# Optimization experiments

Hardware: AMD Instinct MI355X
Metric: run time of the kernel (lower is better)

The kernel has to match this reference:

```python
import jax, jax.numpy as jnp
import numpy as np

D, DFFN, H, P, L = 256, 1024, 8, 4, 4
B, LQ = 32, 300
LENS = [2048, 1024, 512, 256]
STARTS = [0, 2048, 3072, 3584]
S = sum(LENS)


def setup_inputs() -> dict:
    key = jax.random.key(0)
    ks = iter(jax.random.split(key, 64))
    def W(shape, s=0.02):
        return jax.random.normal(next(ks), shape, jnp.float32) * s
    inp = {}
    inp['tgt'] = W((B, LQ, D), 1.0)
    inp['query_pos'] = W((B, LQ, D), 1.0)
    centers = jax.random.uniform(next(ks), (B, LQ, L))
    widths = 0.05 + 0.2 * jax.random.uniform(next(ks), (B, LQ, L))
    inp['reference_points'] = jnp.stack([centers, widths], -1)  # (B,Lq,L,2) = (center,width)
    inp['src'] = W((B, S, D), 1.0)
    inp['temporal_lengths'] = np.array(LENS, np.int64)
    inp['level_start_index'] = np.array(STARTS, np.int64)
    for n, shape in [('sa_qw', (D, D)), ('sa_kw', (D, D)), ('sa_vw', (D, D)), ('sa_ow', (D, D)), ('ff1_w', (D, DFFN)), ('ff2_w', (DFFN, D))]:
        inp[n] = W(shape)
    for n, sz in [('sa_qb', D), ('sa_kb', D), ('sa_vb', D), ('sa_ob', D), ('ff1_b', DFFN), ('ff2_b', D)]:
        inp[n] = jnp.zeros((sz,), jnp.float32)
    for pre in ['ca', 'se']:
        inp[pre + '_off_w'] = W((D, H * L * P))
        inp[pre + '_off_b'] = jnp.zeros((H * L * P,), jnp.float32)
        inp[pre + '_attn_w'] = W((D, H * L * P))
        inp[pre + '_attn_b'] = jnp.zeros((H * L * P,), jnp.float32)
        inp[pre + '_val_w'] = W((D, D))
        inp[pre + '_val_b'] = jnp.zeros((D,), jnp.float32)
        inp[pre + '_out_w'] = W((D, D))
        inp[pre + '_out_b'] = jnp.zeros((D,), jnp.float32)
    for n in ['ln1', 'lnse', 'ln2', 'ln3']:
        inp[n + '_g'] = jnp.ones((D,), jnp.float32)
        inp[n + '_b'] = jnp.zeros((D,), jnp.float32)
    return inp


def _ln(x, g, b, eps=1e-5):
    m = jnp.mean(x, -1, keepdims=True)
    v = jnp.mean((x - m) ** 2, -1, keepdims=True)
    return (x - m) * jax.lax.rsqrt(v + eps) * g + b


def _mha(q, k, v, qw, qb, kw, kb, vw, vb, ow, ob):
    b, lq, d = q.shape
    dh = d // H
    qh = (q @ qw + qb).reshape(b, lq, H, dh).transpose(0, 2, 1, 3)
    kh = (k @ kw + kb).reshape(b, -1, H, dh).transpose(0, 2, 1, 3)
    vh = (v @ vw + vb).reshape(b, -1, H, dh).transpose(0, 2, 1, 3)
    scores = jnp.einsum('bhqd,bhkd->bhqk', qh, kh) * (dh ** -0.5)
    attn = jax.nn.softmax(scores, -1)
    out = jnp.einsum('bhqk,bhkd->bhqd', attn, vh).transpose(0, 2, 1, 3).reshape(b, lq, d)
    return out @ ow + ob


def _deform(q, ref, src, lens, starts, vw, vb, offw, offb, aw, ab, ow, ob, boundary):
    b, lq, d = q.shape
    dh = d // H
    value = (src @ vw + vb).reshape(b, -1, H, dh)  # (B,S,H,Dh)
    off = (q @ offw + offb).reshape(b, lq, H, L, P)
    attn = jax.nn.softmax((q @ aw + ab).reshape(b, lq, H, L * P), -1).reshape(b, lq, H, L, P)
    center = ref[..., 0][:, :, None, :, None]  # (B,Lq,1,L,1)
    width = ref[..., 1][:, :, None, :, None]
    if boundary:
        # half the points anchored at segment start, half at segment end
        sign = jnp.where(jnp.arange(P) < P // 2, -0.5, 0.5)
        anchor = center + sign * width
    else:
        anchor = center
    loc = anchor + off / P * width * 0.5  # normalized sampling locations (B,Lq,H,L,P)
    out = jnp.zeros((b, lq, H, dh), value.dtype)
    for l in range(L):
        T = int(lens[l]); s0 = int(starts[l])
        v = value[:, s0:s0 + T].transpose(0, 2, 1, 3)  # (B,H,T,Dh)
        x = loc[:, :, :, l, :] * T - 0.5  # align_corners=False grid
        x0 = jnp.floor(x)
        w = x - x0
        i0 = x0.astype(jnp.int32)
        i1 = i0 + 1
        m0 = ((i0 >= 0) & (i0 < T)).astype(v.dtype)
        m1 = ((i1 >= 0) & (i1 < T)).astype(v.dtype)
        i0c = jnp.clip(i0, 0, T - 1)
        i1c = jnp.clip(i1, 0, T - 1)
        def gather(idx):
            idxh = idx.transpose(0, 2, 1, 3).reshape(b, H, lq * P, 1)
            g = jnp.take_along_axis(v, jnp.broadcast_to(idxh, (b, H, lq * P, dh)), axis=2)
            return g.reshape(b, H, lq, P, dh).transpose(0, 2, 1, 3, 4)  # (B,Lq,H,P,Dh)
        samp = gather(i0c) * ((1 - w) * m0)[..., None] + gather(i1c) * (w * m1)[..., None]
        out = out + jnp.einsum('bqhp,bqhpd->bqhd', attn[:, :, :, l, :], samp)
    return out.reshape(b, lq, d) @ ow + ob


def reference(tgt, query_pos, reference_points, src, temporal_lengths, level_start_index,
              sa_qw, sa_qb, sa_kw, sa_kb, sa_vw, sa_vb, sa_ow, sa_ob,
              ca_off_w, ca_off_b, ca_attn_w, ca_attn_b, ca_val_w, ca_val_b, ca_out_w, ca_out_b,
              se_off_w, se_off_b, se_attn_w, se_attn_b, se_val_w, se_val_b, se_out_w, se_out_b,
              ff1_w, ff1_b, ff2_w, ff2_b,
              ln1_g, ln1_b, lnse_g, lnse_b, ln2_g, ln2_b, ln3_g, ln3_b):
    lens = np.asarray(temporal_lengths)
    starts = np.asarray(level_start_index)
    q = tgt + query_pos
    t2 = _mha(q, q, tgt, sa_qw, sa_qb, sa_kw, sa_kb, sa_vw, sa_vb, sa_ow, sa_ob)
    tgt = _ln(tgt + t2, ln2_g, ln2_b)
    t2 = _deform(tgt + query_pos, reference_points, src, lens, starts,
                 ca_val_w, ca_val_b, ca_off_w, ca_off_b, ca_attn_w, ca_attn_b, ca_out_w, ca_out_b, False)
    tgt = _ln(tgt + t2, ln1_g, ln1_b)
    t2 = _deform(tgt + query_pos, reference_points, src, lens, starts,
                 se_val_w, se_val_b, se_off_w, se_off_b, se_attn_w, se_attn_b, se_out_w, se_out_b, True)
    tgt = _ln(tgt + t2, lnse_g, lnse_b)
    t2 = jax.nn.relu(tgt @ ff1_w + ff1_b) @ ff2_w + ff2_b
    tgt = _ln(tgt + t2, ln3_g, ln3_b)
    return tgt
```

## Files before the change

kernel.cpp:

```cpp
#include <hip/hip_runtime.h>
#include <hip/hip_bf16.h>

namespace {

typedef unsigned short u16;
typedef unsigned int u32;

constexpr int D    = 256;
constexpr int H    = 8;
constexpr int DH   = 32;
constexpr int L    = 4;
constexpr int P    = 4;
constexpr int B    = 32;
constexpr int LQ   = 300;
constexpr int NQ   = B * LQ;
constexpr int S    = 3840;
constexpr int MS   = B * S;
constexpr int DFFN = 1024;

typedef __attribute__((ext_vector_type(8))) short bf16x8;
typedef __attribute__((ext_vector_type(4))) float f32x4;

__device__ inline u16 f2b(float x) {
  u32 u = __builtin_bit_cast(u32, x);
  u32 r = (u + 0x7FFFu + ((u >> 16) & 1u)) >> 16;
  return (u16)r;
}
__device__ inline u32 pk2(float a, float b) {
  return (u32)f2b(a) | ((u32)f2b(b) << 16);
}
__device__ inline void unpack2(u32 w, float& a, float& b) {
  a = __builtin_bit_cast(float, w << 16);
  b = __builtin_bit_cast(float, w & 0xffff0000u);
}

template<bool OUT_BF16, bool RELU>
__global__ __launch_bounds__(256) void gemm_sm(
    const u16* __restrict__ A, const u16* __restrict__ Bt,
    const float* __restrict__ bias, void* __restrict__ Cv,
    int M, int K, int N)
{
  constexpr int BM = 64, BN = 64, BK = 64, LDK = 72;
  __shared__ __align__(16) u16 sh[(BM + BN) * LDK];
  u16* As = sh;
  u16* Bs = sh + BM * LDK;
  const int tid  = threadIdx.x;
  const int lane = tid & 63;
  const int wid  = tid >> 6;
  const int wm = wid >> 1, wn = wid & 1;
  const int m0 = blockIdx.y * BM, n0 = blockIdx.x * BN;

  f32x4 acc[2][2] = {};
  uint4 ra[2], rb[2];
  const int NT = K / BK;
  const int srow = tid >> 3, sch = (tid & 7) * 8;

#pragma unroll
  for (int i = 0; i < 2; ++i) {
    const int row = srow + i * 32;
    ra[i] = *(const uint4*)(A  + (size_t)(m0 + row) * K + sch);
    rb[i] = *(const uint4*)(Bt + (size_t)(n0 + row) * K + sch);
  }

  for (int t = 0; t < NT; ++t) {
#pragma unroll
    for (int i = 0; i < 2; ++i) {
      const int row = srow + i * 32;
      *(uint4*)(&As[row * LDK + sch]) = ra[i];
      *(uint4*)(&Bs[row * LDK + sch]) = rb[i];
    }
    __syncthreads();
    if (t + 1 < NT) {
      const int k0 = (t + 1) * BK;
#pragma unroll
      for (int i = 0; i < 2; ++i) {
        const int row = srow + i * 32;
        ra[i] = *(const uint4*)(A  + (size_t)(m0 + row) * K + k0 + sch);
        rb[i] = *(const uint4*)(Bt + (size_t)(n0 + row) * K + k0 + sch);
      }
    }
#pragma unroll
    for (int kk = 0; kk < 2; ++kk) {
      const int krd = kk * 32 + (lane >> 4) * 8;
      bf16x8 af[2], bf[2];
#pragma unroll
      for (int m = 0; m < 2; ++m)
        af[m] = *(const bf16x8*)(&As[(wm * 32 + (lane & 15) + 16 * m) * LDK + krd]);
#pragma unroll
      for (int n = 0; n < 2; ++n)
        bf[n] = *(const bf16x8*)(&Bs[(wn * 32 + (lane & 15) + 16 * n) * LDK + krd]);
#pragma unroll
      for (int m = 0; m < 2; ++m)
#pragma unroll
        for (int n = 0; n < 2; ++n)
          acc[m][n] = __builtin_amdgcn_mfma_f32_16x16x32_bf16(af[m], bf[n], acc[m][n], 0, 0, 0);
    }
    __syncthreads();
  }

  const int cr = (lane >> 4) * 4;
  const int cc = lane & 15;
  if constexpr (OUT_BF16) {
    u16* stg = sh;
#pragma unroll
    for (int n = 0; n < 2; ++n) {
      const int lc = wn * 32 + n * 16 + cc;
      const float bv = bias[n0 + lc];
#pragma unroll
      for (int m = 0; m < 2; ++m) {
        const int lr0 = wm * 32 + m * 16 + cr;
#pragma unroll
        for (int r = 0; r < 4; ++r) {
          float x = acc[m][n][r] + bv;
          if (RELU) x = fmaxf(x, 0.f);
          stg[(lr0 + r) * LDK + lc] = f2b(x);
        }
      }
    }
    __syncthreads();
    u16* Cb = (u16*)Cv;
#pragma unroll
    for (int i = 0; i < 2; ++i) {
      const int c = tid + 256 * i;
      const int row = c >> 3, ch = c & 7;
      *(uint4*)(Cb + (size_t)(m0 + row) * N + n0 + ch * 8) =
          *(const uint4*)(&stg[row * LDK + ch * 8]);
    }
  } else {
#pragma unroll
    for (int n = 0; n < 2; ++n) {
      const int gc = n0 + wn * 32 + n * 16 + cc;
      const float bv = bias[gc];
#pragma unroll
      for (int m = 0; m < 2; ++m) {
        const int gr0 = m0 + wm * 32 + m * 16 + cr;
#pragma unroll
        for (int r = 0; r < 4; ++r) {
          float x = acc[m][n][r] + bv;
          if (RELU) x = fmaxf(x, 0.f);
          ((float*)Cv)[(size_t)(gr0 + r) * N + gc] = x;
        }
      }
    }
  }
}

__global__ __launch_bounds__(256) void gemm_qkv(
    const u16* __restrict__ qbuf, const u16* __restrict__ tgtb,
    const u16* __restrict__ saqk_t, const u16* __restrict__ sav_t,
    const float* __restrict__ qkb, const float* __restrict__ vbias,
    u16* __restrict__ qkbuf, u16* __restrict__ vh)
{
  constexpr int K = 256, BK = 64, LDK = 72;
  __shared__ __align__(16) u16 sh[128 * LDK];
  u16* As = sh;
  u16* Bs = sh + 64 * LDK;
  const bool isv = blockIdx.x >= 8;
  const u16* A  = isv ? tgtb : qbuf;
  const u16* Bt = isv ? sav_t : saqk_t;
  const float* bias = isv ? vbias : qkb;
  u16* C = isv ? vh : qkbuf;
  const int N = isv ? 256 : 512;
  const int n0 = (isv ? (int)blockIdx.x - 8 : (int)blockIdx.x) * 64;
  const int m0 = blockIdx.y * 64;

  const int tid  = threadIdx.x;
  const int lane = tid & 63;
  const int wid  = tid >> 6;
  const int wm = wid >> 1, wn = wid & 1;

  f32x4 acc[2][2] = {};
  uint4 ra[2], rb[2];
  const int srow = tid >> 3, sch = (tid & 7) * 8;

#pragma unroll
  for (int i = 0; i < 2; ++i) {
    const int row = srow + i * 32;
    ra[i] = *(const uint4*)(A  + (size_t)(m0 + row) * K + sch);
    rb[i] = *(const uint4*)(Bt + (size_t)(n0 + row) * K + sch);
  }
  for (int t = 0; t < 4; ++t) {
#pragma unroll
    for (int i = 0; i < 2; ++i) {
      const int row = srow + i * 32;
      *(uint4*)(&As[row * LDK + sch]) = ra[i];
      *(uint4*)(&Bs[row * LDK + sch]) = rb[i];
    }
    __syncthreads();
    if (t + 1 < 4) {
      const int k0 = (t + 1) * BK;
#pragma unroll
      for (int i = 0; i < 2; ++i) {
        const int row = srow + i * 32;
        ra[i] = *(const uint4*)(A  + (size_t)(m0 + row) * K + k0 + sch);
        rb[i] = *(const uint4*)(Bt + (size_t)(n0 + row) * K + k0 + sch);
      }
    }
#pragma unroll
    for (int kk = 0; kk < 2; ++kk) {
      const int krd = kk * 32 + (lane >> 4) * 8;
      bf16x8 af[2], bf[2];
#pragma unroll
      for (int m = 0; m < 2; ++m)
        af[m] = *(const bf16x8*)(&As[(wm * 32 + (lane & 15) + 16 * m) * LDK + krd]);
#pragma unroll
      for (int n = 0; n < 2; ++n)
        bf[n] = *(const bf16x8*)(&Bs[(wn * 32 + (lane & 15) + 16 * n) * LDK + krd]);
#pragma unroll
      for (int m = 0; m < 2; ++m)
#pragma unroll
        for (int n = 0; n < 2; ++n)
          acc[m][n] = __builtin_amdgcn_mfma_f32_16x16x32_bf16(af[m], bf[n], acc[m][n], 0, 0, 0);
    }
    __syncthreads();
  }

  const int cr = (lane >> 4) * 4;
  const int cc = lane & 15;
  u16* stg = sh;
#pragma unroll
  for (int n = 0; n < 2; ++n) {
    const int lc = wn * 32 + n * 16 + cc;
    const float bv = bias[n0 + lc];
#pragma unroll
    for (int m = 0; m < 2; ++m) {
      const int lr0 = wm * 32 + m * 16 + cr;
#pragma unroll
      for (int r = 0; r < 4; ++r)
        stg[(lr0 + r) * LDK + lc] = f2b(acc[m][n][r] + bv);
    }
  }
  __syncthreads();
#pragma unroll
  for (int i = 0; i < 2; ++i) {
    const int c = tid + 256 * i;
    const int row = c >> 3, ch = c & 7;
    *(uint4*)(C + (size_t)(m0 + row) * N + n0 + ch * 8) =
        *(const uint4*)(&stg[row * LDK + ch * 8]);
  }
}

__global__ __launch_bounds__(512) void gemm_val4(
    const float* __restrict__ A, const u16* __restrict__ Bt2,
    const float* __restrict__ bias2, u16* __restrict__ Vca, u16* __restrict__ Vse)
{
  __shared__ __align__(16) char shraw[33792];
  char* Asw = shraw;
  const int tid  = threadIdx.x;
  const int lane = tid & 63;
  const int w    = tid >> 6;
  const int nh   = blockIdx.x & 1;
  const int m0   = (blockIdx.x >> 1) * 64;
  u16* dst = nh ? Vse : Vca;
  const u16* Bt = Bt2 + nh * 256 * 256;
  const float* bias = bias2 + nh * 256;

#pragma unroll
  for (int i = 0; i < 4; ++i) {
    const int idx = tid + 512 * i;
    const int row = idx >> 5, ch = idx & 31;
    const float* ap = A + (size_t)(m0 + row) * 256 + ch * 8;
    const float4 f0 = *(const float4*)(ap);
    const float4 f1 = *(const float4*)(ap + 4);
    uint4 pk;
    pk.x = pk2(f0.x, f0.y); pk.y = pk2(f0.z, f0.w);
    pk.z = pk2(f1.x, f1.y); pk.w = pk2(f1.z, f1.w);
    *(uint4*)(Asw + row * 512 + ((ch * 16) ^ ((row & 7) << 4))) = pk;
  }
  __syncthreads();

  f32x4 acc[4][2] = {};
  const u16* bb = Bt + (size_t)(w * 32 + (lane & 15)) * 256 + (lane >> 4) * 8;
  bf16x8 bcur[2], bnxt[2];
#pragma unroll
  for (int n = 0; n < 2; ++n) bcur[n] = *(const bf16x8*)(bb + n * 4096);

#pragma unroll
  for (int kk = 0; kk < 8; ++kk) {
    bf16x8 af[4];
    const int kb = kk * 64 + (lane >> 4) * 16;
#pragma unroll
    for (int m = 0; m < 4; ++m) {
      const int row = m * 16 + (lane & 15);
      af[m] = *(const bf16x8*)(Asw + row * 512 + (kb ^ ((row & 7) << 4)));
    }
    if (kk < 7) {
#pragma unroll
      for (int n = 0; n < 2; ++n)
        bnxt[n] = *(const bf16x8*)(bb + n * 4096 + (kk + 1) * 32);
    }
#pragma unroll
    for (int m = 0; m < 4; ++m)
#pragma unroll
      for (int n = 0; n < 2; ++n)
        acc[m][n] = __builtin_amdgcn_mfma_f32_16x16x32_bf16(af[m], bcur[n], acc[m][n], 0, 0, 0);
#pragma unroll
    for (int n = 0; n < 2; ++n) bcur[n] = bnxt[n];
  }
  __syncthreads();

  constexpr int STC = 264;
  u16* stg = (u16*)shraw;
  const int cr = (lane >> 4) * 4;
  const int cc = lane & 15;
#pragma unroll
  for (int n = 0; n < 2; ++n) {
    const int col = w * 32 + n * 16 + cc;
    const float bv = bias[col];
#pragma unroll
    for (int m = 0; m < 4; ++m) {
      const int r0 = m * 16 + cr;
#pragma unroll
      for (int r = 0; r < 4; ++r)
        stg[(r0 + r) * STC + col] = f2b(acc[m][n][r] + bv);
    }
  }
  __syncthreads();
#pragma unroll
  for (int i = 0; i < 4; ++i) {
    const int c = tid + 512 * i;
    const int row = c >> 5, ch = c & 31;
    *(uint4*)(dst + (size_t)(m0 + row) * 256 + ch * 8) =
        *(const uint4*)(&stg[row * STC + ch * 8]);
  }
}

template<int MODE>
__global__ __launch_bounds__(1024) void gemm_ln(
    const u16* __restrict__ A, const u16* __restrict__ Bt,
    const float* __restrict__ bias, const float* __restrict__ res,
    const float* __restrict__ g, const float* __restrict__ be,
    const float* __restrict__ qpos,
    float* __restrict__ fout, u16* __restrict__ bfout, int K)
{
  constexpr int BK = 64, LDK = 72;
  __shared__ __align__(16) float ftile[64 * 264];
  u16* As = (u16*)ftile;
  u16* Bs = As + 64 * LDK;
  const int tid  = threadIdx.x;
  const int lane = tid & 63;
  const int wid  = tid >> 6;
  const int wm = wid >> 2, wn = wid & 3;
  const int m0 = blockIdx.x * 64;

  f32x4 acc[4] = {};
  const int NT = K / BK;
  const bool am = tid < 512;
  const int arow = tid >> 3, ach = (tid & 7) * 8;

  uint4 ra = {};
  uint4 rb[2];
  if (am) ra = *(const uint4*)(A + (size_t)(m0 + arow) * K + ach);
#pragma unroll
  for (int i = 0; i < 2; ++i) {
    const int idx = tid + 1024 * i;
    const int brow = idx >> 3, bch = (idx & 7) * 8;
    rb[i] = *(const uint4*)(Bt + (size_t)brow * K + bch);
  }

  for (int t = 0; t < NT; ++t) {
    if (am) *(uint4*)(&As[arow * LDK + ach]) = ra;
#pragma unroll
    for (int i = 0; i < 2; ++i) {
      const int idx = tid + 1024 * i;
      const int brow = idx >> 3, bch = (idx & 7) * 8;
      *(uint4*)(&Bs[brow * LDK + bch]) = rb[i];
    }
    __syncthreads();
    if (t + 1 < NT) {
      const int k0 = (t + 1) * BK;
      if (am) ra = *(const uint4*)(A + (size_t)(m0 + arow) * K + k0 + ach);
#pragma unroll
      for (int i = 0; i < 2; ++i) {
        const int idx = tid + 1024 * i;
        const int brow = idx >> 3, bch = (idx & 7) * 8;
        rb[i] = *(const uint4*)(Bt + (size_t)brow * K + k0 + bch);
      }
    }
#pragma unroll
    for (int kk = 0; kk < 2; ++kk) {
      const int krd = kk * 32 + (lane >> 4) * 8;
      bf16x8 af, bf[4];
      af = *(const bf16x8*)(&As[(wm * 16 + (lane & 15)) * LDK + krd]);
#pragma unroll
      for (int n = 0; n < 4; ++n)
        bf[n] = *(const bf16x8*)(&Bs[(wn * 64 + n * 16 + (lane & 15)) * LDK + krd]);
#pragma unroll
      for (int n = 0; n < 4; ++n)
        acc[n] = __builtin_amdgcn_mfma_f32_16x16x32_bf16(af, bf[n], acc[n], 0, 0, 0);
    }
    __syncthreads();
  }

  const int cr = (lane >> 4) * 4;
  const int cc = lane & 15;
#pragma unroll
  for (int n = 0; n < 4; ++n) {
    const int col = wn * 64 + n * 16 + cc;
    const float bv = bias[col];
#pragma unroll
    for (int r = 0; r < 4; ++r)
      ftile[(wm * 16 + cr + r) * 264 + col] = acc[n][r] + bv;
  }
  __syncthreads();

  const int row = tid >> 4, s16 = tid & 15;
  const size_t grow = (size_t)(m0 + row) * 256;
  float vv[16];
  float sum = 0.f;
#pragma unroll
  for (int j = 0; j < 4; ++j) {
    const int col = s16 * 4 + j * 64;
    const float4 fv = *(const float4*)(&ftile[row * 264 + col]);
    const float4 rv = *(const float4*)(res + grow + col);
    vv[j * 4 + 0] = fv.x + rv.x; vv[j * 4 + 1] = fv.y + rv.y;
    vv[j * 4 + 2] = fv.z + rv.z; vv[j * 4 + 3] = fv.w + rv.w;
    sum += vv[j * 4 + 0] + vv[j * 4 + 1] + vv[j * 4 + 2] + vv[j * 4 + 3];
  }
  sum += __shfl_xor(sum, 1, 64);
  sum += __shfl_xor(sum, 2, 64);
  sum += __shfl_xor(sum, 4, 64);
  sum += __shfl_xor(sum, 8, 64);
  const float mean = sum * (1.f / 256.f);
  float sq = 0.f;
#pragma unroll
  for (int k = 0; k < 16; ++k) { const float d = vv[k] - mean; sq += d * d; }
  sq += __shfl_xor(sq, 1, 64);
  sq += __shfl_xor(sq, 2, 64);
  sq += __shfl_xor(sq, 4, 64);
  sq += __shfl_xor(sq, 8, 64);
  const float rstd = rsqrtf(sq * (1.f / 256.f) + 1e-5f);

#pragma unroll
  for (int j = 0; j < 4; ++j) {
    const int col = s16 * 4 + j * 64;
    const float4 gv = *(const float4*)(g + col);
    const float4 bv = *(const float4*)(be + col);
    float4 y;
    y.x = (vv[j * 4 + 0] - mean) * rstd * gv.x + bv.x;
    y.y = (vv[j * 4 + 1] - mean) * rstd * gv.y + bv.y;
    y.z = (vv[j * 4 + 2] - mean) * rstd * gv.z + bv.z;
    y.w = (vv[j * 4 + 3] - mean) * rstd * gv.w + bv.w;
    *(float4*)(fout + grow + col) = y;
    if constexpr (MODE == 0) {
      const float4 qv = *(const float4*)(qpos + grow + col);
      uint2 pk;
      pk.x = pk2(y.x + qv.x, y.y + qv.y);
      pk.y = pk2(y.z + qv.z, y.w + qv.w);
      *(uint2*)(bfout + grow + col) = pk;
    } else if constexpr (MODE == 1) {
      uint2 pk;
      pk.x = pk2(y.x, y.y);
      pk.y = pk2(y.z, y.w);
      *(uint2*)(bfout + grow + col) = pk;
    }
  }
}

struct WSpec { const float* w; u16* wt; int K, N, blk0; };
struct WPack { WSpec s[14]; };

struct PrepArgs {
  const float *ca_off_b, *ca_attn_b, *se_off_b, *se_attn_b;
  const float *sa_qb, *sa_kb, *ca_val_b, *se_val_b;
  float *bias4, *qkb, *valb;
  const float *tgt, *qpos;
  u16 *tgtb, *qbuf;
  int n4, nwt;
};

__global__ __launch_bounds__(256) void prep_all(WPack p, PrepArgs a) {
  __shared__ float tile[32][33];
  const int b = blockIdx.x;
  if (b < a.nwt) {
    int i = 0;
#pragma unroll
    for (int j = 1; j < 14; ++j) if (b >= p.s[j].blk0) i = j;
    const float* w = p.s[i].w;
    u16* wt = p.s[i].wt;
    const int K = p.s[i].K, N = p.s[i].N;
    const int lb = b - p.s[i].blk0;
    const int ntN = N >> 5;
    const int tk = lb / ntN, tn = lb - tk * ntN;
    const int r = threadIdx.x >> 5, c = threadIdx.x & 31;
#pragma unroll
    for (int j = 0; j < 4; ++j)
      tile[r + j * 8][c] = w[(size_t)(tk * 32 + r + j * 8) * N + tn * 32 + c];
    __syncthreads();
#pragma unroll
    for (int j = 0; j < 4; ++j)
      wt[(size_t)(tn * 32 + r + j * 8) * K + tk * 32 + c] = f2b(tile[c][r + j * 8]);
  } else if (b == a.nwt) {
#pragma unroll
    for (int u = 0; u < 2; ++u) {
      const int t = threadIdx.x + 256 * u;
      a.bias4[t] = t < 128 ? a.ca_off_b[t] : t < 256 ? a.ca_attn_b[t - 128]
                 : t < 384 ? a.se_off_b[t - 256] : a.se_attn_b[t - 384];
      a.qkb[t]  = t < 256 ? a.sa_qb[t] : a.sa_kb[t - 256];
      a.valb[t] = t < 256 ? a.ca_val_b[t] : a.se_val_b[t - 256];
    }
  } else {
    const int i = (b - a.nwt - 1) * 256 + threadIdx.x;
    if (i < a.n4) {
      const float4 t = ((const float4*)a.tgt)[i];
      const float4 q = ((const float4*)a.qpos)[i];
      uint2 x, y;
      x.x = pk2(t.x, t.y); x.y = pk2(t.z, t.w);
      y.x = pk2(t.x + q.x, t.y + q.y); y.y = pk2(t.z + q.z, t.w + q.w);
      ((uint2*)a.tgtb)[i] = x;
      ((uint2*)a.qbuf)[i] = y;
    }
  }
}

__global__ __launch_bounds__(512) void mha_v2(
    const u16* __restrict__ qk, const u16* __restrict__ vh,
    u16* __restrict__ out)
{
  __shared__ __align__(16) float Ks[8 * 300 * 4];
  __shared__ __align__(16) float Vs[8 * 300 * 4];
  const int bh  = blockIdx.x & 255;
  const int seg = blockIdx.x >> 8;
  const int b = bh >> 3, h = bh & 7;
  const u16* kbase = qk + (size_t)b * LQ * 512 + 256 + h * DH;
  const u16* vbase = vh + (size_t)b * LQ * D + h * DH;
  for (int e = threadIdx.x; e < 300 * 8; e += 512) {
    const int r = e >> 3, j = e & 7;
    float4 f;
    const uint2 kv = *(const uint2*)(kbase + (size_t)r * 512 + j * 4);
    unpack2(kv.x, f.x, f.y);
    unpack2(kv.y, f.z, f.w);
    *(float4*)(&Ks[(j * 300 + r) * 4]) = f;
    const uint2 vv = *(const uint2*)(vbase + (size_t)r * D + j * 4);
    unpack2(vv.x, f.x, f.y);
    unpack2(vv.y, f.z, f.w);
    *(float4*)(&Vs[(j * 300 + r) * 4]) = f;
  }
  __syncthreads();

  const int lane = threadIdx.x & 63;
  const int lq = (threadIdx.x >> 6) * 16 + (lane >> 2);
  const int kc = lane & 3;
  const int q = seg * 128 + lq;
  if (q >= LQ) return;

  const u16* qrow = qk + (size_t)(b * LQ + q) * 512 + h * DH;
  float qv[DH];
#pragma unroll
  for (int c4 = 0; c4 < 4; ++c4) {
    const uint4 u = *(const uint4*)(qrow + c4 * 8);
    unpack2(u.x, qv[c4 * 8 + 0], qv[c4 * 8 + 1]);
    unpack2(u.y, qv[c4 * 8 + 2], qv[c4 * 8 + 3]);
    unpack2(u.z, qv[c4 * 8 + 4], qv[c4 * 8 + 5]);
    unpack2(u.w, qv[c4 * 8 + 6], qv[c4 * 8 + 7]);
  }
#pragma unroll
  for (int d = 0; d < DH; ++d) qv[d] *= 0.17677669529663689f;

  float o[DH] = {};
  float ssum = 0.f;
  const float* kp = &Ks[kc * 75 * 4];
  const float* vp = &Vs[kc * 75 * 4];
  for (int i = 0; i < 75; ++i) {
    float s = 0.f;
#pragma unroll
    for (int j = 0; j < 8; ++j) {
      const float4 kf = *(const float4*)(kp + i * 4 + j * 1200);
      s += qv[j * 4 + 0] * kf.x + qv[j * 4 + 1] * kf.y
         + qv[j * 4 + 2] * kf.z + qv[j * 4 + 3] * kf.w;
    }
    const float p = __expf(s);
    ssum += p;
#pragma unroll
    for (int j = 0; j < 8; ++j) {
      const float4 vf = *(const float4*)(vp + i * 4 + j * 1200);
      o[j * 4 + 0] += p * vf.x; o[j * 4 + 1] += p * vf.y;
      o[j * 4 + 2] += p * vf.z; o[j * 4 + 3] += p * vf.w;
    }
  }

  ssum += __shfl_xor(ssum, 1, 64);
  ssum += __shfl_xor(ssum, 2, 64);
#pragma unroll
  for (int d = 0; d < DH; ++d) {
    o[d] += __shfl_xor(o[d], 1, 64);
    o[d] += __shfl_xor(o[d], 2, 64);
  }
  const float inv = 1.f / ssum;

  u16* orow = out + (size_t)(b * LQ + q) * D + h * DH;
#pragma unroll
  for (int c = 0; c < 4; ++c) {
    if (kc == c) {
      uint4 w;
      w.x = pk2(o[c * 8 + 0] * inv, o[c * 8 + 1] * inv);
      w.y = pk2(o[c * 8 + 2] * inv, o[c * 8 + 3] * inv);
      w.z = pk2(o[c * 8 + 4] * inv, o[c * 8 + 5] * inv);
      w.w = pk2(o[c * 8 + 6] * inv, o[c * 8 + 7] * inv);
      *(uint4*)(orow + c * 8) = w;
    }
  }
}

template<bool BOUNDARY>
__global__ __launch_bounds__(512) void deform_v2(
    const float* __restrict__ oa, const float* __restrict__ ref,
    const u16* __restrict__ value, u16* __restrict__ out)
{
  __shared__ __align__(16) uint4 owt[4][128];
  const int unit = threadIdx.x >> 7;
  const int bq = blockIdx.x * 4 + unit;
  const int b = bq / LQ;
  const int t = threadIdx.x & 127;
  const int h = t >> 4;
  const int l = (t >> 2) & 3;
  const int p = t & 3;

  const float off   = oa[(size_t)bq * 256 + t];
  const float logit = oa[(size_t)bq * 256 + 128 + t];
  const float center = ref[(size_t)bq * 8 + l * 2 + 0];
  const float width  = ref[(size_t)bq * 8 + l * 2 + 1];

  const float e = __expf(logit);
  float ssum = e;
  ssum += __shfl_xor(ssum, 1, 64);
  ssum += __shfl_xor(ssum, 2, 64);
  ssum += __shfl_xor(ssum, 4, 64);
  ssum += __shfl_xor(ssum, 8, 64);
  const float wa = e / ssum;

  const int T  = 2048 >> l;
  const int s0 = 4096 - (4096 >> l);
  float anchor = center;
  if (BOUNDARY) anchor += (p < 2 ? -0.5f : 0.5f) * width;
  const float loc = anchor + off * width * 0.125f;
  const float x = loc * (float)T - 0.5f;
  const float x0 = floorf(x);
  const float w = x - x0;
  const int i0 = (int)x0;
  const int i1 = i0 + 1;
  const float w0 = (i0 >= 0 && i0 < T) ? wa * (1.f - w) : 0.f;
  const float w1 = (i1 >= 0 && i1 < T) ? wa * w : 0.f;
  const int i0c = min(max(i0, 0), T - 1);
  const int i1c = min(max(i1, 0), T - 1);
  uint4 pack;
  pack.x = (u32)((s0 + i0c) * (D * 2) + h * (DH * 2));
  pack.y = __builtin_bit_cast(u32, w0);
  pack.z = (u32)((s0 + i1c) * (D * 2) + h * (DH * 2));
  pack.w = __builtin_bit_cast(u32, w1);
  owt[unit][t] = pack;
  __syncthreads();

  const int g  = t >> 4;
  const int ln = t & 15;
  const char* vb = (const char*)(value + (size_t)b * S * D) + ln * 4;
  float o0 = 0.f, o1 = 0.f;
#pragma unroll
  for (int j = 0; j < 16; ++j) {
    const uint4 ow = owt[unit][g * 16 + j];
    const u32 v0 = *(const u32*)(vb + ow.x);
    const u32 v1 = *(const u32*)(vb + ow.z);
    const float wt0 = __builtin_bit_cast(float, ow.y);
    const float wt1 = __builtin_bit_cast(float, ow.w);
    float a, c;
    unpack2(v0, a, c); o0 += wt0 * a; o1 += wt0 * c;
    unpack2(v1, a, c); o0 += wt1 * a; o1 += wt1 * c;
  }
  const u32 res = pk2(o0, o1);
  *(u32*)(out + (size_t)bq * D + g * DH + ln * 2) = res;
}

}

extern "C" void kernel_launch(void* const* d_in, const int* in_sizes, int n_in,
                              void* d_out, int out_size, void* d_ws, size_t ws_size,
                              hipStream_t stream)
{
  const float* tgt   = (const float*)d_in[0];
  const float* qpos  = (const float*)d_in[1];
  const float* ref   = (const float*)d_in[2];
  const float* src   = (const float*)d_in[3];
  const float* sa_qw = (const float*)d_in[6];
  const float* sa_kw = (const float*)d_in[7];
  const float* sa_vw = (const float*)d_in[8];
  const float* sa_ow = (const float*)d_in[9];
  const float* ff1_w = (const float*)d_in[10];
  const float* ff2_w = (const float*)d_in[11];
  const float* sa_qb = (const float*)d_in[12];
  const float* sa_kb = (const float*)d_in[13];
  const float* sa_vb = (const float*)d_in[14];
  const float* sa_ob = (const float*)d_in[15];
  const float* ff1_b = (const float*)d_in[16];
  const float* ff2_b = (const float*)d_in[17];
  const float* ca_off_w  = (const float*)d_in[18];
  const float* ca_off_b  = (const float*)d_in[19];
  const float* ca_attn_w = (const float*)d_in[20];
  const float* ca_attn_b = (const float*)d_in[21];
  const float* ca_val_w  = (const float*)d_in[22];
  const float* ca_val_b  = (const float*)d_in[23];
  const float* ca_out_w  = (const float*)d_in[24];
  const float* ca_out_b  = (const float*)d_in[25];
  const float* se_off_w  = (const float*)d_in[26];
  const float* se_off_b  = (const float*)d_in[27];
  const float* se_attn_w = (const float*)d_in[28];
  const float* se_attn_b = (const float*)d_in[29];
  const float* se_val_w  = (const float*)d_in[30];
  const float* se_val_b  = (const float*)d_in[31];
  const float* se_out_w  = (const float*)d_in[32];
  const float* se_out_b  = (const float*)d_in[33];
  const float* ln1_g  = (const float*)d_in[34];
  const float* ln1_b  = (const float*)d_in[35];
  const float* lnse_g = (const float*)d_in[36];
  const float* lnse_b = (const float*)d_in[37];
  const float* ln2_g  = (const float*)d_in[38];
  const float* ln2_b  = (const float*)d_in[39];
  const float* ln3_g  = (const float*)d_in[40];
  const float* ln3_b  = (const float*)d_in[41];

  const size_t ND = (size_t)NQ * D;
  const size_t MD = (size_t)MS * D;

  char* base = (char*)d_ws;
  size_t off = 0;
  auto alloc = [&](size_t bytes) -> void* {
    void* p = base + off;
    off += (bytes + 255) & ~(size_t)255;
    return p;
  };
  u16*  Vca  = (u16*)alloc(MD * 2);
  u16*  Vse  = (u16*)alloc(MD * 2);
  u16*  qkbuf = (u16*)alloc((size_t)NQ * 512 * 2);
  u16*  vh   = (u16*)alloc(ND * 2);
  u16*  qbuf = (u16*)alloc(ND * 2);
  u16*  smpb = (u16*)alloc(ND * 2);
  u16*  tgtb = (u16*)alloc(ND * 2);
  u16*  curb = (u16*)alloc(ND * 2);
  float* cur = (float*)alloc(ND * 4);
  float* oabuf = (float*)alloc((size_t)NQ * 256 * 4);
  float* bias4 = (float*)alloc(512 * 4);
  float* qkb   = (float*)alloc(512 * 4);
  float* valb  = (float*)alloc(512 * 4);

  u16* ffh = Vca;

  WPack pk;
  int wi = 0, blk = 0;
  auto addw = [&](const float* w, int K, int N) -> u16* {
    u16* wt = (u16*)alloc((size_t)K * N * 2);
    pk.s[wi].w = w; pk.s[wi].wt = wt; pk.s[wi].K = K; pk.s[wi].N = N; pk.s[wi].blk0 = blk;
    blk += (K / 32) * (N / 32);
    ++wi;
    return wt;
  };
  u16* saq_t = addw(sa_qw, D, D);
  u16* sak_t = addw(sa_kw, D, D);        (void)sak_t;
  u16* sav_t = addw(sa_vw, D, D);
  u16* sao_t = addw(sa_ow, D, D);
  u16* ff1_t = addw(ff1_w, D, DFFN);
  u16* ff2_t = addw(ff2_w, DFFN, D);
  u16* caoff_t = addw(ca_off_w, D, 128);
  u16* caatt_t = addw(ca_attn_w, D, 128);  (void)caatt_t;
  u16* seoff_t = addw(se_off_w, D, 128);
  u16* seatt_t = addw(se_attn_w, D, 128);  (void)seatt_t;
  u16* caval_t = addw(ca_val_w, D, D);
  u16* seval_t = addw(se_val_w, D, D);     (void)seval_t;
  u16* caout_t = addw(ca_out_w, D, D);
  u16* seout_t = addw(se_out_w, D, D);

  const int n4 = (int)(ND / 4);

  PrepArgs pa;
  pa.ca_off_b = ca_off_b; pa.ca_attn_b = ca_attn_b;
  pa.se_off_b = se_off_b; pa.se_attn_b = se_attn_b;
  pa.sa_qb = sa_qb; pa.sa_kb = sa_kb; pa.ca_val_b = ca_val_b; pa.se_val_b = se_val_b;
  pa.bias4 = bias4; pa.qkb = qkb; pa.valb = valb;
  pa.tgt = tgt; pa.qpos = qpos; pa.tgtb = tgtb; pa.qbuf = qbuf;
  pa.n4 = n4; pa.nwt = blk;
  prep_all<<<blk + 1 + 2400, 256, 0, stream>>>(pk, pa);

  gemm_val4<<<(MS / 64) * 2, 512, 0, stream>>>(src, caval_t, valb, Vca, Vse);

  gemm_qkv<<<dim3(12, 150), 256, 0, stream>>>(qbuf, tgtb, saq_t, sav_t, qkb, sa_vb, qkbuf, vh);
  mha_v2<<<B * H * 3, 512, 0, stream>>>(qkbuf, vh, smpb);
  gemm_ln<0><<<NQ / 64, 1024, 0, stream>>>(smpb, sao_t, sa_ob, tgt, ln2_g, ln2_b, qpos, cur, qbuf, D);

  gemm_sm<false, false><<<dim3(4, 150), 256, 0, stream>>>(qbuf, caoff_t, bias4, oabuf, NQ, D, 256);
  deform_v2<false><<<NQ / 4, 512, 0, stream>>>(oabuf, ref, Vca, smpb);
  gemm_ln<0><<<NQ / 64, 1024, 0, stream>>>(smpb, caout_t, ca_out_b, cur, ln1_g, ln1_b, qpos, cur, qbuf, D);

  gemm_sm<false, false><<<dim3(4, 150), 256, 0, stream>>>(qbuf, seoff_t, bias4 + 256, oabuf, NQ, D, 256);
  deform_v2<true><<<NQ / 4, 512, 0, stream>>>(oabuf, ref, Vse, smpb);
  gemm_ln<1><<<NQ / 64, 1024, 0, stream>>>(smpb, seout_t, se_out_b, cur, lnse_g, lnse_b, nullptr, cur, curb, D);

  gemm_sm<true,  true ><<<dim3(16, 150), 256, 0, stream>>>(curb, ff1_t, ff1_b, ffh, NQ, D, DFFN);
  gemm_ln<2><<<NQ / 64, 1024, 0, stream>>>(ffh, ff2_t, ff2_b, cur, ln3_g, ln3_b, nullptr, (float*)d_out, nullptr, DFFN);
}
```

Baseline: 474.0 us.

## Widen deform gathers to 16-byte loads and shrink value GEMM tiles

The deformable sampling kernel now gives each lane one 16-byte chunk of a value row for a quarter of the sample points, instead of a 4-byte load for every point. Partial sums are then combined with cross-lane shuffles, which cuts the number of gather instructions. Separately, the value-projection GEMM moves to 32-row tiles with 256 threads, each wave covering 64 columns, to raise block count and occupancy. The trade-offs are extra shuffle-reduction work and idle lanes at the store in the deform kernel, plus more B-matrix reloads per output in the GEMM.

```diff
diff --git a/kernel.cpp b/kernel.cpp
--- a/kernel.cpp
+++ b/kernel.cpp
@@ -9,8 +9,6 @@
 constexpr int D    = 256;
 constexpr int H    = 8;
 constexpr int DH   = 32;
-constexpr int L    = 4;
-constexpr int P    = 4;
 constexpr int B    = 32;
 constexpr int LQ   = 300;
 constexpr int NQ   = B * LQ;
@@ -240,24 +238,24 @@
   }
 }
 
-__global__ __launch_bounds__(512) void gemm_val4(
+__global__ __launch_bounds__(256) void gemm_val5(
     const float* __restrict__ A, const u16* __restrict__ Bt2,
     const float* __restrict__ bias2, u16* __restrict__ Vca, u16* __restrict__ Vse)
 {
-  __shared__ __align__(16) char shraw[33792];
+  __shared__ __align__(16) char shraw[16896];
   char* Asw = shraw;
   const int tid  = threadIdx.x;
   const int lane = tid & 63;
   const int w    = tid >> 6;
   const int nh   = blockIdx.x & 1;
-  const int m0   = (blockIdx.x >> 1) * 64;
+  const int m0   = (blockIdx.x >> 1) * 32;
   u16* dst = nh ? Vse : Vca;
   const u16* Bt = Bt2 + nh * 256 * 256;
   const float* bias = bias2 + nh * 256;
 
 #pragma unroll
   for (int i = 0; i < 4; ++i) {
-    const int idx = tid + 512 * i;
+    const int idx = tid + 256 * i;
     const int row = idx >> 5, ch = idx & 31;
     const float* ap = A + (size_t)(m0 + row) * 256 + ch * 8;
     const float4 f0 = *(const float4*)(ap);
@@ -269,33 +267,33 @@
   }
   __syncthreads();
 
-  f32x4 acc[4][2] = {};
-  const u16* bb = Bt + (size_t)(w * 32 + (lane & 15)) * 256 + (lane >> 4) * 8;
-  bf16x8 bcur[2], bnxt[2];
-#pragma unroll
-  for (int n = 0; n < 2; ++n) bcur[n] = *(const bf16x8*)(bb + n * 4096);
+  f32x4 acc[2][4] = {};
+  const u16* bb = Bt + (size_t)(w * 64 + (lane & 15)) * 256 + (lane >> 4) * 8;
+  bf16x8 bcur[4], bnxt[4];
+#pragma unroll
+  for (int n = 0; n < 4; ++n) bcur[n] = *(const bf16x8*)(bb + n * 4096);
 
 #pragma unroll
   for (int kk = 0; kk < 8; ++kk) {
-    bf16x8 af[4];
+    bf16x8 af[2];
     const int kb = kk * 64 + (lane >> 4) * 16;
 #pragma unroll
-    for (int m = 0; m < 4; ++m) {
+    for (int m = 0; m < 2; ++m) {
       const int row = m * 16 + (lane & 15);
       af[m] = *(const bf16x8*)(Asw + row * 512 + (kb ^ ((row & 7) << 4)));
     }
     if (kk < 7) {
 #pragma unroll
-      for (int n = 0; n < 2; ++n)
+      for (int n = 0; n < 4; ++n)
         bnxt[n] = *(const bf16x8*)(bb + n * 4096 + (kk + 1) * 32);
     }
 #pragma unroll
-    for (int m = 0; m < 4; ++m)
-#pragma unroll
-      for (int n = 0; n < 2; ++n)
+    for (int m = 0; m < 2; ++m)
+#pragma unroll
+      for (int n = 0; n < 4; ++n)
         acc[m][n] = __builtin_amdgcn_mfma_f32_16x16x32_bf16(af[m], bcur[n], acc[m][n], 0, 0, 0);
 #pragma unroll
-    for (int n = 0; n < 2; ++n) bcur[n] = bnxt[n];
+    for (int n = 0; n < 4; ++n) bcur[n] = bnxt[n];
   }
   __syncthreads();
 
@@ -304,11 +302,11 @@
   const int cr = (lane >> 4) * 4;
   const int cc = lane & 15;
 #pragma unroll
-  for (int n = 0; n < 2; ++n) {
-    const int col = w * 32 + n * 16 + cc;
+  for (int n = 0; n < 4; ++n) {
+    const int col = w * 64 + n * 16 + cc;
     const float bv = bias[col];
 #pragma unroll
-    for (int m = 0; m < 4; ++m) {
+    for (int m = 0; m < 2; ++m) {
       const int r0 = m * 16 + cr;
 #pragma unroll
       for (int r = 0; r < 4; ++r)
@@ -318,7 +316,7 @@
   __syncthreads();
 #pragma unroll
   for (int i = 0; i < 4; ++i) {
-    const int c = tid + 512 * i;
+    const int c = tid + 256 * i;
     const int row = c >> 5, ch = c & 31;
     *(uint4*)(dst + (size_t)(m0 + row) * 256 + ch * 8) =
         *(const uint4*)(&stg[row * STC + ch * 8]);
@@ -603,7 +601,7 @@
 }
 
 template<bool BOUNDARY>
-__global__ __launch_bounds__(512) void deform_v2(
+__global__ __launch_bounds__(512) void deform_v3(
     const float* __restrict__ oa, const float* __restrict__ ref,
     const u16* __restrict__ value, u16* __restrict__ out)
 {
@@ -653,21 +651,34 @@
 
   const int g  = t >> 4;
   const int ln = t & 15;
-  const char* vb = (const char*)(value + (size_t)b * S * D) + ln * 4;
-  float o0 = 0.f, o1 = 0.f;
-#pragma unroll
-  for (int j = 0; j < 16; ++j) {
-    const uint4 ow = owt[unit][g * 16 + j];
-    const u32 v0 = *(const u32*)(vb + ow.x);
-    const u32 v1 = *(const u32*)(vb + ow.z);
-    const float wt0 = __builtin_bit_cast(float, ow.y);
-    const float wt1 = __builtin_bit_cast(float, ow.w);
-    float a, c;
-    unpack2(v0, a, c); o0 += wt0 * a; o1 += wt0 * c;
-    unpack2(v1, a, c); o0 += wt1 * a; o1 += wt1 * c;
-  }
-  const u32 res = pk2(o0, o1);
-  *(u32*)(out + (size_t)bq * D + g * DH + ln * 2) = res;
+  const int qd = ln & 3;
+  const int ts = ln >> 2;
+  const char* vb = (const char*)(value + (size_t)b * S * D) + qd * 16;
+  float o[8] = {};
+#pragma unroll
+  for (int i = 0; i < 8; ++i) {
+    const int rowidx = i * 4 + ts;
+    const uint4 ow = owt[unit][g * 16 + (rowidx >> 1)];
+    const u32 boff = (rowidx & 1) ? ow.z : ow.x;
+    const float wt = __builtin_bit_cast(float, (rowidx & 1) ? ow.w : ow.y);
+    const uint4 v = *(const uint4*)(vb + boff);
+    float a0, a1;
+    unpack2(v.x, a0, a1); o[0] += wt * a0; o[1] += wt * a1;
+    unpack2(v.y, a0, a1); o[2] += wt * a0; o[3] += wt * a1;
+    unpack2(v.z, a0, a1); o[4] += wt * a0; o[5] += wt * a1;
+    unpack2(v.w, a0, a1); o[6] += wt * a0; o[7] += wt * a1;
+  }
+#pragma unroll
+  for (int d = 0; d < 8; ++d) {
+    o[d] += __shfl_xor(o[d], 4, 64);
+    o[d] += __shfl_xor(o[d], 8, 64);
+  }
+  if (ts == 0) {
+    uint4 wv;
+    wv.x = pk2(o[0], o[1]); wv.y = pk2(o[2], o[3]);
+    wv.z = pk2(o[4], o[5]); wv.w = pk2(o[6], o[7]);
+    *(uint4*)(out + (size_t)bq * D + g * DH + qd * 8) = wv;
+  }
 }
 
 }
@@ -778,18 +789,18 @@
   pa.n4 = n4; pa.nwt = blk;
   prep_all<<<blk + 1 + 2400, 256, 0, stream>>>(pk, pa);
 
-  gemm_val4<<<(MS / 64) * 2, 512, 0, stream>>>(src, caval_t, valb, Vca, Vse);
+  gemm_val5<<<(MS / 32) * 2, 256, 0, stream>>>(src, caval_t, valb, Vca, Vse);
 
   gemm_qkv<<<dim3(12, 150), 256, 0, stream>>>(qbuf, tgtb, saq_t, sav_t, qkb, sa_vb, qkbuf, vh);
   mha_v2<<<B * H * 3, 512, 0, stream>>>(qkbuf, vh, smpb);
   gemm_ln<0><<<NQ / 64, 1024, 0, stream>>>(smpb, sao_t, sa_ob, tgt, ln2_g, ln2_b, qpos, cur, qbuf, D);
 
   gemm_sm<false, false><<<dim3(4, 150), 256, 0, stream>>>(qbuf, caoff_t, bias4, oabuf, NQ, D, 256);
-  deform_v2<false><<<NQ / 4, 512, 0, stream>>>(oabuf, ref, Vca, smpb);
+  deform_v3<false><<<NQ / 4, 512, 0, stream>>>(oabuf, ref, Vca, smpb);
   gemm_ln<0><<<NQ / 64, 1024, 0, stream>>>(smpb, caout_t, ca_out_b, cur, ln1_g, ln1_b, qpos, cur, qbuf, D);
 
   gemm_sm<false, false><<<dim3(4, 150), 256, 0, stream>>>(qbuf, seoff_t, bias4 + 256, oabuf, NQ, D, 256);
-  deform_v2<true><<<NQ / 4, 512, 0, stream>>>(oabuf, ref, Vse, smpb);
+  deform_v3<true><<<NQ / 4, 512, 0, stream>>>(oabuf, ref, Vse, smpb);
   gemm_ln<1><<<NQ / 64, 1024, 0, stream>>>(smpb, seout_t, se_out_b, cur, lnse_g, lnse_b, nullptr, cur, curb, D);
 
   gemm_sm<true,  true ><<<dim3(16, 150), 256, 0, stream>>>(curb, ff1_t, ff1_b, ffh, NQ, D, DFFN);
```

Result: slower. 524.7 us (+10.7%).
